# Kernel optimization log

Hardware: AMD Instinct MI355X
Metric: run time of the kernel (lower is better)

## Reference

```python
import jax, jax.numpy as jnp
import numpy as np

B, N, D = 8, 2048, 512


def setup_inputs() -> dict:
    key = jax.random.key(0)
    ks = jax.random.split(key, 16)
    s = 1.0 / np.sqrt(D)  # ~ torch Linear default init scale
    inp = {
        "X": jax.random.normal(ks[0], (B, N, D), jnp.float32),
        "Y": jax.random.normal(ks[1], (B, N, D), jnp.float32),
    }
    names = ["xq", "xk", "xv", "yq", "yk", "yv"]
    for i, nm in enumerate(names):
        inp[f"W_{nm}"] = jax.random.uniform(ks[2 + 2 * i], (D, D), jnp.float32, -s, s)
        inp[f"b_{nm}"] = jax.random.uniform(ks[3 + 2 * i], (D,), jnp.float32, -s, s)
    return inp


def _lin(x, W, b):
    # torch nn.Linear: x @ W^T + b
    return jnp.einsum("bnd,ed->bne", x, W) + b


def reference(X, Y, W_xq, b_xq, W_xk, b_xk, W_xv, b_xv, W_yq, b_yq, W_yk, b_yk, W_yv, b_yv):
    d = X.shape[-1]
    scale = 1.0 / jnp.sqrt(jnp.asarray(d, X.dtype))
    Q1, K1, V1 = _lin(X, W_xq, b_xq), _lin(X, W_xk, b_xk), _lin(X, W_xv, b_xv)
    Q2, K2, V2 = _lin(Y, W_yq, b_yq), _lin(Y, W_yk, b_yk), _lin(Y, W_yv, b_yv)
    # NOTE: F.softmax called without dim on a 3-D tensor -> torch legacy dim=0 (batch axis).
    S1 = jnp.einsum("bnd,bmd->bnm", Q1, K2) * scale  # [B, N, N]
    A1 = jax.nn.softmax(S1, axis=0)
    U_A1 = X + jnp.einsum("bnm,bmd->bnd", A1, V2)  # dropout = identity (eval)
    S2 = jnp.einsum("bnd,bmd->bnm", Q2, K1) * scale
    A2 = jax.nn.softmax(S2, axis=0)
    U_A2 = Y + jnp.einsum("bnm,bmd->bnd", A2, V1)
    return U_A1 + U_A2
```

## Files before the change

### kernel.cpp

```cpp
#include <hip/hip_runtime.h>

typedef unsigned short u16;
typedef unsigned char u8;
typedef __attribute__((ext_vector_type(8))) short bf16x8;
typedef __attribute__((ext_vector_type(4))) float f32x4;
typedef __attribute__((ext_vector_type(8))) u16 u16x8;
typedef __attribute__((ext_vector_type(2))) int i32x2;
typedef __attribute__((ext_vector_type(2))) float f32x2;

#define GLOAD_LDS(g, s) __builtin_amdgcn_global_load_lds( \
    (const __attribute__((address_space(1))) void*)(g),   \
    (__attribute__((address_space(3))) void*)(s), 16, 0, 0)

__device__ __forceinline__ u16 f2bf(float f) {
  union { float f; unsigned u; } v; v.f = f;
  unsigned r = v.u + 0x7fffu + ((v.u >> 16) & 1u);
  return (u16)(r >> 16);
}
__device__ __forceinline__ float bf2f(u16 h) {
  union { unsigned u; float f; } v; v.u = ((unsigned)h) << 16;
  return v.f;
}

__device__ __forceinline__ unsigned lds_addr(const void* p) {
  return (unsigned)(unsigned long long)(__attribute__((address_space(3))) const void*)p;
}
__device__ __forceinline__ bf16x8 ds128(const void* p) {
  bf16x8 r;
  asm volatile("ds_read_b128 %0, %1" : "=v"(r) : "v"(lds_addr(p)));
  return r;
}
__device__ __forceinline__ i32x2 ds64(const void* p) {
  i32x2 r;
  asm volatile("ds_read_b64 %0, %1" : "=v"(r) : "v"(lds_addr(p)));
  return r;
}
__device__ __forceinline__ bf16x8 cvt8(i32x2 v) {
  f32x2 f0 = __builtin_amdgcn_cvt_pk_f32_fp8(v[0], false);
  f32x2 f1 = __builtin_amdgcn_cvt_pk_f32_fp8(v[0], true);
  f32x2 f2 = __builtin_amdgcn_cvt_pk_f32_fp8(v[1], false);
  f32x2 f3 = __builtin_amdgcn_cvt_pk_f32_fp8(v[1], true);
  unsigned w0, w1, w2, w3;
  asm("v_cvt_pk_bf16_f32 %0, %1, %2" : "=v"(w0) : "v"(f0[0]), "v"(f0[1]));
  asm("v_cvt_pk_bf16_f32 %0, %1, %2" : "=v"(w1) : "v"(f1[0]), "v"(f1[1]));
  asm("v_cvt_pk_bf16_f32 %0, %1, %2" : "=v"(w2) : "v"(f2[0]), "v"(f2[1]));
  asm("v_cvt_pk_bf16_f32 %0, %1, %2" : "=v"(w3) : "v"(f3[0]), "v"(f3[1]));
  union { unsigned w[4]; bf16x8 v8; } u;
  u.w[0] = w0; u.w[1] = w1; u.w[2] = w2; u.w[3] = w3;
  return u.v8;
}

__device__ __forceinline__ void stage_pair(const u16* gA, int lda, const u16* gB, int ldb,
                                           u16* lA, u16* lB, int wave, int lane) {
  int row = (wave << 4) + (lane >> 2);
  int kb  = (lane & 3) << 3;
  GLOAD_LDS(gA + row * lda + kb,        lA + (wave << 9));
  GLOAD_LDS(gA + (row + 64) * lda + kb, lA + ((wave + 4) << 9));
  GLOAD_LDS(gB + row * ldb + kb,        lB + (wave << 9));
  GLOAD_LDS(gB + (row + 64) * ldb + kb, lB + ((wave + 4) << 9));
}

__device__ __forceinline__ void gemm_seg(f32x4 (&acc)[4][4],
    const u16* Ag, const u16* Bg, int lda, int ldb, int nk,
    u16* As, u16* Bs, int wave, int lane) {
  const int wr = (wave >> 1) << 6, wc = (wave & 1) << 6;
  const int rl = lane & 15, rk = (lane >> 4) << 3;
  stage_pair(Ag, lda, Bg, ldb, As, Bs, wave, lane);
  if (nk > 1)
    stage_pair(Ag + 32, lda, Bg + 32, ldb, As + 4096, Bs + 4096, wave, lane);
  int bufsel = 0;
  for (int kt = 0; kt < nk; ++kt) {
    if (kt + 1 < nk) asm volatile("s_waitcnt vmcnt(4)" ::: "memory");
    else             asm volatile("s_waitcnt vmcnt(0)" ::: "memory");
    __builtin_amdgcn_s_barrier();
    asm volatile("" ::: "memory");
    if (kt + 2 < nk) {
      int nb = bufsel + 2; if (nb >= 3) nb -= 3;
      stage_pair(Ag + (long)(kt + 2) * 32, lda, Bg + (long)(kt + 2) * 32, ldb,
                 As + nb * 4096, Bs + nb * 4096, wave, lane);
    }
    const u16* ab = As + bufsel * 4096;
    const u16* bb = Bs + bufsel * 4096;
    bf16x8 af[4], bfr[4];
#pragma unroll
    for (int i = 0; i < 4; i++)
      af[i]  = *(const bf16x8*)(ab + ((wr + (i << 4) + rl) << 5) + rk);
#pragma unroll
    for (int j = 0; j < 4; j++)
      bfr[j] = *(const bf16x8*)(bb + ((wc + (j << 4) + rl) << 5) + rk);
#pragma unroll
    for (int i = 0; i < 4; i++)
#pragma unroll
      for (int j = 0; j < 4; j++)
        acc[i][j] = __builtin_amdgcn_mfma_f32_16x16x32_bf16(af[i], bfr[j], acc[i][j], 0, 0, 0);
    __builtin_amdgcn_sched_barrier(0);
    bufsel = bufsel + 1; if (bufsel == 3) bufsel = 0;
  }
}

__device__ __forceinline__ void stage_one(const u16* g, int ld, u16* d, int tid) {
  int rw = tid >> 3;
  int gs = ((tid & 7) ^ (rw & 7)) << 3;
  int wb = (tid >> 6) << 9;
#pragma unroll
  for (int p = 0; p < 4; p++)
    GLOAD_LDS(g + (long)(p * 64 + rw) * ld + gs, d + p * 4096 + wb);
}

__device__ __forceinline__ void gemm256d(f32x4 (&acc)[8][4],
    const u16* Ag, int lda, const u16* Bg, int ldb, int nk,
    u16* As, u16* Bs, int tid) {
  const int lane = tid & 63, wid = tid >> 6;
  const int wr = (wid >> 2) << 7;
  const int wc = (wid & 3) << 6;
  const int rl = lane & 15, kg = lane >> 4;
  const int swz0 = (kg ^ (rl & 7)) << 3;
  const int rbA = (wr + rl) * 64, rbB = (wc + rl) * 64;

  stage_one(Ag, lda, As, tid);
  stage_one(Bg, ldb, Bs, tid);
  if (nk > 1) stage_one(Ag + 64, lda, As + 16384, tid);

  int ba = 0;
  for (int t = 0; t < nk; ++t) {
    if (t + 1 < nk) asm volatile("s_waitcnt vmcnt(4)" ::: "memory");
    else            asm volatile("s_waitcnt vmcnt(0)" ::: "memory");
    __builtin_amdgcn_s_barrier();
    if (t + 1 < nk)
      stage_one(Bg + (t + 1) * 64, ldb, Bs + ((t + 1) & 1) * 16384, tid);
    if (t + 2 < nk) {
      int nb = ba + 2; if (nb >= 3) nb -= 3;
      stage_one(Ag + (long)(t + 2) * 64, lda, As + nb * 16384, tid);
    }
    const u16* ab = As + ba * 16384 + rbA;
    const u16* bb = Bs + (t & 1) * 16384 + rbB;
#pragma unroll
    for (int kk = 0; kk < 2; kk++) {
      const int sw = swz0 ^ (kk << 5);
      bf16x8 a[8], b[4];
#pragma unroll
      for (int i = 0; i < 8; i++) a[i] = ds128(ab + i * 1024 + sw);
#pragma unroll
      for (int j = 0; j < 4; j++) b[j] = ds128(bb + j * 1024 + sw);
      asm volatile("s_waitcnt lgkmcnt(0)" ::: "memory");
      __builtin_amdgcn_sched_barrier(0);
      __builtin_amdgcn_s_setprio(1);
#pragma unroll
      for (int i = 0; i < 8; i++)
#pragma unroll
        for (int j = 0; j < 4; j++)
          acc[i][j] = __builtin_amdgcn_mfma_f32_16x16x32_bf16(a[i], b[j], acc[i][j], 0, 0, 0);
      __builtin_amdgcn_s_setprio(0);
      __builtin_amdgcn_sched_barrier(0);
    }
    ba = ba + 1; if (ba == 3) ba = 0;
  }
}

__device__ __forceinline__ void stage_pv(const u8* gA, const u16* gB,
                                         u8* Ad, u8* Bd, int tid) {
  int w = tid >> 6;
#pragma unroll
  for (int pass = 0; pass < 2; pass++) {
    int gid = pass * 512 + tid;
    int ra = gid >> 2, ga = gid & 3;
    GLOAD_LDS(gA + (long)ra * 2048 + ((ga ^ (ra & 3)) << 4),
              Ad + pass * 8192 + w * 1024);
    int rb = gid >> 3, gb = gid & 7;
    GLOAD_LDS(gB + (long)rb * 2048 + ((gb ^ (rb & 7)) << 3),
              Bd + pass * 8192 + w * 1024);
  }
}

__device__ __forceinline__ void gemm_pv8(f32x4 (&acc)[4][4],
    const u8* Ag, const u16* Bg, u8* As, u8* Bs, int tid) {
  const int lane = tid & 63, wid = tid >> 6;
  const int mq = wid >> 1, nh = wid & 1;
  const int rl = lane & 15, kg = lane >> 4;
  const int nk = 32;

  stage_pv(Ag, Bg, As, Bs, tid);
  stage_pv(Ag + 64, Bg + 64, As + 16384, Bs + 16384, tid);
  int bsel = 0;
  for (int t = 0; t < nk; ++t) {
    if (t + 1 < nk) asm volatile("s_waitcnt vmcnt(4)" ::: "memory");
    else            asm volatile("s_waitcnt vmcnt(0)" ::: "memory");
    __builtin_amdgcn_s_barrier();
    if (t + 2 < nk) {
      int nb = bsel + 2; if (nb >= 3) nb -= 3;
      stage_pv(Ag + (long)(t + 2) * 64, Bg + (t + 2) * 64,
               As + nb * 16384, Bs + nb * 16384, tid);
    }
    const u8* ab = As + bsel * 16384 + (mq * 64 + rl) * 64 + ((kg & 1) << 3);
    const u8* bb = Bs + bsel * 16384 + (nh * 64 + rl) * 128;
#pragma unroll
    for (int kk = 0; kk < 2; kk++) {
      const int sa = (((kk << 1) + (kg >> 1)) ^ (rl & 3)) << 4;
      const int sb = (((kk << 2) + kg) ^ (rl & 7)) << 4;
      i32x2 ar[4]; bf16x8 bfr[4];
#pragma unroll
      for (int i = 0; i < 4; i++) ar[i] = ds64(ab + i * 1024 + sa);
#pragma unroll
      for (int j = 0; j < 4; j++) bfr[j] = ds128(bb + j * 2048 + sb);
      asm volatile("s_waitcnt lgkmcnt(0)" ::: "memory");
      __builtin_amdgcn_sched_barrier(0);
      bf16x8 a[4];
#pragma unroll
      for (int i = 0; i < 4; i++) a[i] = cvt8(ar[i]);
      __builtin_amdgcn_s_setprio(1);
#pragma unroll
      for (int i = 0; i < 4; i++)
#pragma unroll
        for (int j = 0; j < 4; j++)
          acc[i][j] = __builtin_amdgcn_mfma_f32_16x16x32_bf16(a[i], bfr[j], acc[i][j], 0, 0, 0);
      __builtin_amdgcn_s_setprio(0);
      __builtin_amdgcn_sched_barrier(0);
    }
    bsel = bsel + 1; if (bsel == 3) bsel = 0;
  }
}

__global__ __launch_bounds__(256) void k_cvt2(const float* __restrict__ inX,
                                              const float* __restrict__ inY,
                                              u16* __restrict__ oX, u16* __restrict__ oY,
                                              int n8) {
  int i = blockIdx.x * 256 + threadIdx.x;
  const float* in = (i < n8) ? inX : inY;
  u16* out = (i < n8) ? oX : oY;
  int k = (i < n8) ? i : i - n8;
  const float4* pf = (const float4*)in + (long)k * 2;
  float4 a = pf[0], b = pf[1];
  u16x8 o;
  o[0] = f2bf(a.x); o[1] = f2bf(a.y); o[2] = f2bf(a.z); o[3] = f2bf(a.w);
  o[4] = f2bf(b.x); o[5] = f2bf(b.y); o[6] = f2bf(b.z); o[7] = f2bf(b.w);
  *((u16x8*)out + k) = o;
}

struct P6 { const float* p[6]; };
struct O6 { u16* p[6]; };

__global__ __launch_bounds__(256) void k_cvt_w(P6 w, u16* __restrict__ out) {
  int z = blockIdx.y;
  int i = blockIdx.x * 256 + threadIdx.x;
  const float4* pf = (const float4*)w.p[z] + (long)i * 2;
  float4 a = pf[0], b = pf[1];
  u16x8 o;
  o[0] = f2bf(a.x); o[1] = f2bf(a.y); o[2] = f2bf(a.z); o[3] = f2bf(a.w);
  o[4] = f2bf(b.x); o[5] = f2bf(b.y); o[6] = f2bf(b.z); o[7] = f2bf(b.w);
  *((u16x8*)(out + (long)z * 262144) + i) = o;
}

__global__ __launch_bounds__(256) void k_proj(const u16* __restrict__ Xb, const u16* __restrict__ Yb,
                                              const u16* __restrict__ Wb, P6 bias, O6 dst) {
  __shared__ u16 As[12288], Bs[12288];
  int x = blockIdx.x;
  int swz = (x & 7) * 384 + (x >> 3);
  int bm = swz / 24;
  int r  = swz - bm * 24;
  int z = r >> 2, bn = r & 3;
  int tid = threadIdx.x, wave = tid >> 6, lane = tid & 63;
  const u16* Ag = (z < 3 ? Xb : Yb) + (long)bm * 128 * 512;
  const u16* Bg = Wb + (long)z * 262144 + (long)bn * 128 * 512;
  f32x4 acc[4][4] = {};
  gemm_seg(acc, Ag, Bg, 512, 512, 16, As, Bs, wave, lane);
  const float* bi = bias.p[z];
  u16* D = dst.p[z];
  int wr = (wave >> 1) << 6, wc = (wave & 1) << 6;
  int row0 = bm * 128 + wr + ((lane >> 4) << 2);
  int col0 = bn * 128 + wc + (lane & 15);
  float bj[4];
#pragma unroll
  for (int j = 0; j < 4; j++) bj[j] = bi[col0 + (j << 4)];
#pragma unroll
  for (int i = 0; i < 4; i++)
#pragma unroll
    for (int j = 0; j < 4; j++)
#pragma unroll
      for (int rr = 0; rr < 4; rr++)
        D[(long)(row0 + (i << 4) + rr) * 512 + col0 + (j << 4)] = f2bf(acc[i][j][rr] + bj[j]);
}

__global__ __launch_bounds__(512) void k_s(const u16* __restrict__ Q, const u16* __restrict__ K,
                                           u16* __restrict__ S) {
  __shared__ u16 As[49152], Bs[32768];
  int x = blockIdx.x;
  int swz = (x & 7) * 64 + (x >> 3);
  int bn = swz & 7, bm = (swz >> 3) & 7, b = swz >> 6;
  int tid = threadIdx.x;
  const u16* Ag = Q + (long)b * 1048576 + (long)bm * 256 * 512;
  const u16* Bg = K + (long)b * 1048576 + (long)bn * 256 * 512;
  f32x4 acc[8][4] = {};
  gemm256d(acc, Ag, 512, Bg, 512, 8, As, Bs, tid);
  u16* D = S + (long)b * 4194304;
  const float scale = 0.04419417382415922f;
  int lane = tid & 63, wid = tid >> 6;
  int row0 = bm * 256 + ((wid >> 2) << 7) + ((lane >> 4) << 2);
  int col0 = bn * 256 + ((wid & 3) << 6) + (lane & 15);
#pragma unroll
  for (int i = 0; i < 8; i++)
#pragma unroll
    for (int j = 0; j < 4; j++)
#pragma unroll
      for (int rr = 0; rr < 4; rr++)
        D[(long)(row0 + (i << 4) + rr) * 2048 + col0 + (j << 4)] = f2bf(acc[i][j][rr] * scale);
}

__global__ __launch_bounds__(256) void k_softmax8(const u16* __restrict__ S,
                                                  u8* __restrict__ A8) {
  int idx = blockIdx.x * 256 + threadIdx.x;
  u16x8 v[8];
#pragma unroll
  for (int b = 0; b < 8; b++) v[b] = *((const u16x8*)(S + (long)b * 4194304) + idx);
  unsigned w0[8], w1[8];
#pragma unroll
  for (int jp = 0; jp < 4; jp++) {
    float va[8], vb[8];
    {
      float e[8], m = -1e30f;
#pragma unroll
      for (int b = 0; b < 8; b++) { e[b] = bf2f(v[b][2 * jp]); m = fmaxf(m, e[b]); }
      float s = 0.f;
#pragma unroll
      for (int b = 0; b < 8; b++) { e[b] = __expf(e[b] - m); s += e[b]; }
      float inv = 1.0f / s;
#pragma unroll
      for (int b = 0; b < 8; b++) va[b] = e[b] * inv;
    }
    {
      float e[8], m = -1e30f;
#pragma unroll
      for (int b = 0; b < 8; b++) { e[b] = bf2f(v[b][2 * jp + 1]); m = fmaxf(m, e[b]); }
      float s = 0.f;
#pragma unroll
      for (int b = 0; b < 8; b++) { e[b] = __expf(e[b] - m); s += e[b]; }
      float inv = 1.0f / s;
#pragma unroll
      for (int b = 0; b < 8; b++) vb[b] = e[b] * inv;
    }
#pragma unroll
    for (int b = 0; b < 8; b++) {
      if (jp == 0)      w0[b] = __builtin_amdgcn_cvt_pk_fp8_f32(va[b], vb[b], 0,     false);
      else if (jp == 1) w0[b] = __builtin_amdgcn_cvt_pk_fp8_f32(va[b], vb[b], w0[b], true);
      else if (jp == 2) w1[b] = __builtin_amdgcn_cvt_pk_fp8_f32(va[b], vb[b], 0,     false);
      else              w1[b] = __builtin_amdgcn_cvt_pk_fp8_f32(va[b], vb[b], w1[b], true);
    }
  }
#pragma unroll
  for (int b = 0; b < 8; b++) {
    i32x2 w; w[0] = (int)w0[b]; w[1] = (int)w1[b];
    *(i32x2*)(A8 + (long)b * 4194304 + (long)idx * 8) = w;
  }
}

__global__ __launch_bounds__(256) void k_tr(const u16* __restrict__ V1, const u16* __restrict__ V2,
                                            u16* __restrict__ T1, u16* __restrict__ T2) {
  __shared__ u16 tile[64][65];
  int z = blockIdx.z;
  const u16* src = (z < 8 ? V1 : V2) + (long)(z & 7) * 1048576;
  u16*       dst = (z < 8 ? T1 : T2) + (long)(z & 7) * 1048576;
  int n0 = blockIdx.x * 64, d0 = blockIdx.y * 64;
  int t = threadIdx.x;
  int r = t >> 2, cs = (t & 3) * 16;
  const u16x8* sp = (const u16x8*)(src + (long)(n0 + r) * 512 + d0 + cs);
  u16x8 a = sp[0], b = sp[1];
#pragma unroll
  for (int jj = 0; jj < 8; jj++) { tile[r][cs + jj] = a[jj]; tile[r][cs + 8 + jj] = b[jj]; }
  __syncthreads();
  u16x8 o0, o1;
#pragma unroll
  for (int jj = 0; jj < 8; jj++) { o0[jj] = tile[cs + jj][r]; o1[jj] = tile[cs + 8 + jj][r]; }
  u16x8* op = (u16x8*)(dst + (long)(d0 + r) * 2048 + n0 + cs);
  op[0] = o0; op[1] = o1;
}

__global__ __launch_bounds__(512) void k_pv8(const u8* __restrict__ A8, const u16* __restrict__ Vt,
                                             const float* __restrict__ X, const float* __restrict__ Y,
                                             float* __restrict__ out, int mode) {
  __shared__ u8 As[49152], Bs[49152];
  int x = blockIdx.x;
  int swz = (x & 7) * 32 + (x >> 3);
  int bn = swz & 3, bm = (swz >> 2) & 7, b = swz >> 5;
  int tid = threadIdx.x;
  const u8*  Ag = A8 + (long)b * 4194304 + (long)bm * 256 * 2048;
  const u16* Bg = Vt + (long)b * 1048576 + (long)bn * 128 * 2048;
  f32x4 acc[4][4] = {};
  gemm_pv8(acc, Ag, Bg, As, Bs, tid);
  int lane = tid & 63, wid = tid >> 6;
  int mq = wid >> 1, nh = wid & 1;
  int row0 = bm * 256 + mq * 64 + ((lane >> 4) << 2);
  int col0 = bn * 128 + nh * 64 + (lane & 15);
  long base = (long)b * 1048576;
#pragma unroll
  for (int i = 0; i < 4; i++)
#pragma unroll
    for (int j = 0; j < 4; j++)
#pragma unroll
      for (int rr = 0; rr < 4; rr++) {
        long idx = base + (long)(row0 + (i << 4) + rr) * 512 + col0 + (j << 4);
        float v = acc[i][j][rr];
        out[idx] = mode ? (out[idx] + v) : (v + X[idx] + Y[idx]);
      }
}

extern "C" void kernel_launch(void* const* d_in, const int* in_sizes, int n_in,
                              void* d_out, int out_size, void* d_ws, size_t ws_size,
                              hipStream_t stream) {
  const float* X = (const float*)d_in[0];
  const float* Y = (const float*)d_in[1];
  P6 wp, bp;
  for (int i = 0; i < 6; i++) { wp.p[i] = (const float*)d_in[2 + 2 * i]; bp.p[i] = (const float*)d_in[3 + 2 * i]; }

  const long NX = 8L * 2048 * 512;
  const long NS = 8L * 2048 * 2048;
  u16* p = (u16*)d_ws;
  u16* Xb = p;  p += NX;
  u16* Yb = p;  p += NX;
  u16* Wb = p;  p += 6L * 512 * 512;
  u16* Q1 = p;  p += NX;
  u16* K2 = p;  p += NX;
  u16* Q2 = p;  p += NX;
  u16* K1 = p;  p += NX;
  u16* Sb = p;  p += NS;
  u16* V1 = Sb;
  u16* V2 = Sb + NX;
  u16* Vt1 = Xb;
  u16* Vt2 = Yb;
  u8* A8_2 = (u8*)Q2;
  u8* A8_1 = (u8*)Q1;
  (void)ws_size; (void)in_sizes; (void)n_in; (void)out_size;

  dim3 T(256);
  k_cvt2<<<dim3(8192), T, 0, stream>>>(X, Y, Xb, Yb, (int)(NX / 8));
  k_cvt_w<<<dim3(128, 6), T, 0, stream>>>(wp, Wb);
  O6 dst; dst.p[0] = Q1; dst.p[1] = K1; dst.p[2] = V1; dst.p[3] = Q2; dst.p[4] = K2; dst.p[5] = V2;
  k_proj<<<dim3(3072), T, 0, stream>>>(Xb, Yb, Wb, bp, dst);
  k_tr<<<dim3(32, 8, 16), T, 0, stream>>>(V1, V2, Vt1, Vt2);
  k_s<<<dim3(512), dim3(512), 0, stream>>>(Q2, K1, Sb);
  k_softmax8<<<dim3(2048), T, 0, stream>>>(Sb, A8_2);
  k_pv8<<<dim3(256), dim3(512), 0, stream>>>(A8_2, Vt1, X, Y, (float*)d_out, 0);
  k_s<<<dim3(512), dim3(512), 0, stream>>>(Q1, K2, Sb);
  k_softmax8<<<dim3(2048), T, 0, stream>>>(Sb, A8_1);
  k_pv8<<<dim3(256), dim3(512), 0, stream>>>(A8_1, Vt2, X, Y, (float*)d_out, 1);
}
```

Measured before the change: 342.3 us.

## Double the PV K-tile and software-pipeline LDS fragment loads in gemm_pv8

The PV GEMM now stages 128-wide K tiles instead of 64, halving the number of main-loop barriers. The fp8 A tile stays triple-buffered, while the V tile moves to double buffering with its own staging call. Inside each K step, LDS fragment reads for the next sub-step are issued before the MFMAs of the current one (register double buffering with a partial lgkmcnt wait), to hide LDS latency. Shared memory grows to 160 KB per block, which limits occupancy to one block per CU, and the vmcnt(4) accounting now has to match a different number of outstanding loads.

```diff
diff --git a/kernel.cpp b/kernel.cpp
--- a/kernel.cpp
+++ b/kernel.cpp
@@ -157,18 +157,20 @@
   }
 }
 
-__device__ __forceinline__ void stage_pv(const u8* gA, const u16* gB,
-                                         u8* Ad, u8* Bd, int tid) {
-  int w = tid >> 6;
-#pragma unroll
-  for (int pass = 0; pass < 2; pass++) {
+__device__ __forceinline__ void stage_A8(const u8* gA, u8* Ad, int tid) {
+#pragma unroll
+  for (int pass = 0; pass < 4; pass++) {
     int gid = pass * 512 + tid;
-    int ra = gid >> 2, ga = gid & 3;
-    GLOAD_LDS(gA + (long)ra * 2048 + ((ga ^ (ra & 3)) << 4),
-              Ad + pass * 8192 + w * 1024);
-    int rb = gid >> 3, gb = gid & 7;
-    GLOAD_LDS(gB + (long)rb * 2048 + ((gb ^ (rb & 7)) << 3),
-              Bd + pass * 8192 + w * 1024);
+    int row = gid >> 3, g = gid & 7;
+    GLOAD_LDS(gA + (long)row * 2048 + ((g ^ (row & 7)) << 4), Ad + (gid << 4));
+  }
+}
+__device__ __forceinline__ void stage_Bv(const u16* gB, u8* Bd, int tid) {
+#pragma unroll
+  for (int pass = 0; pass < 4; pass++) {
+    int gid = pass * 512 + tid;
+    int row = gid >> 4, g = gid & 15;
+    GLOAD_LDS(gB + (long)row * 2048 + ((g ^ (row & 7)) << 3), Bd + (gid << 4));
   }
 }
 
@@ -177,46 +179,62 @@
   const int lane = tid & 63, wid = tid >> 6;
   const int mq = wid >> 1, nh = wid & 1;
   const int rl = lane & 15, kg = lane >> 4;
-  const int nk = 32;
-
-  stage_pv(Ag, Bg, As, Bs, tid);
-  stage_pv(Ag + 64, Bg + 64, As + 16384, Bs + 16384, tid);
-  int bsel = 0;
+  const int nk = 16;
+  const int abase = (mq * 64 + rl) * 128 + ((kg & 1) << 3);
+  const int bbase = (nh * 64 + rl) * 256;
+
+  stage_A8(Ag, As, tid);
+  stage_Bv(Bg, Bs, tid);
+  stage_A8(Ag + 128, As + 32768, tid);
+  int ba = 0;
   for (int t = 0; t < nk; ++t) {
     if (t + 1 < nk) asm volatile("s_waitcnt vmcnt(4)" ::: "memory");
     else            asm volatile("s_waitcnt vmcnt(0)" ::: "memory");
     __builtin_amdgcn_s_barrier();
+    if (t + 1 < nk) stage_Bv(Bg + (t + 1) * 128, Bs + ((t + 1) & 1) * 32768, tid);
     if (t + 2 < nk) {
-      int nb = bsel + 2; if (nb >= 3) nb -= 3;
-      stage_pv(Ag + (long)(t + 2) * 64, Bg + (t + 2) * 64,
-               As + nb * 16384, Bs + nb * 16384, tid);
-    }
-    const u8* ab = As + bsel * 16384 + (mq * 64 + rl) * 64 + ((kg & 1) << 3);
-    const u8* bb = Bs + bsel * 16384 + (nh * 64 + rl) * 128;
-#pragma unroll
-    for (int kk = 0; kk < 2; kk++) {
-      const int sa = (((kk << 1) + (kg >> 1)) ^ (rl & 3)) << 4;
-      const int sb = (((kk << 2) + kg) ^ (rl & 7)) << 4;
-      i32x2 ar[4]; bf16x8 bfr[4];
-#pragma unroll
-      for (int i = 0; i < 4; i++) ar[i] = ds64(ab + i * 1024 + sa);
-#pragma unroll
-      for (int j = 0; j < 4; j++) bfr[j] = ds128(bb + j * 2048 + sb);
-      asm volatile("s_waitcnt lgkmcnt(0)" ::: "memory");
+      int nb = ba + 2; if (nb >= 3) nb -= 3;
+      stage_A8(Ag + (long)(t + 2) * 128, As + nb * 32768, tid);
+    }
+    const u8* ab = As + ba * 32768 + abase;
+    const u8* bb = Bs + (t & 1) * 32768 + bbase;
+    i32x2 ar[2][4]; bf16x8 br[2][4];
+    {
+      const int sa = ((kg >> 1) ^ (rl & 7)) << 4;
+      const int sb = (kg ^ (rl & 7)) << 4;
+#pragma unroll
+      for (int i = 0; i < 4; i++) ar[0][i] = ds64(ab + i * 2048 + sa);
+#pragma unroll
+      for (int j = 0; j < 4; j++) br[0][j] = ds128(bb + j * 4096 + sb);
+    }
+#pragma unroll
+    for (int kk = 0; kk < 4; kk++) {
+      const int cu = kk & 1, nx = cu ^ 1;
+      if (kk < 3) {
+        const int sa = ((((kk + 1) << 1) + (kg >> 1)) ^ (rl & 7)) << 4;
+        const int sb = ((((kk + 1) << 2) + kg) ^ (rl & 7)) << 4;
+#pragma unroll
+        for (int i = 0; i < 4; i++) ar[nx][i] = ds64(ab + i * 2048 + sa);
+#pragma unroll
+        for (int j = 0; j < 4; j++) br[nx][j] = ds128(bb + j * 4096 + sb);
+        asm volatile("s_waitcnt lgkmcnt(8)" ::: "memory");
+      } else {
+        asm volatile("s_waitcnt lgkmcnt(0)" ::: "memory");
+      }
       __builtin_amdgcn_sched_barrier(0);
       bf16x8 a[4];
 #pragma unroll
-      for (int i = 0; i < 4; i++) a[i] = cvt8(ar[i]);
+      for (int i = 0; i < 4; i++) a[i] = cvt8(ar[cu][i]);
       __builtin_amdgcn_s_setprio(1);
 #pragma unroll
       for (int i = 0; i < 4; i++)
 #pragma unroll
         for (int j = 0; j < 4; j++)
-          acc[i][j] = __builtin_amdgcn_mfma_f32_16x16x32_bf16(a[i], bfr[j], acc[i][j], 0, 0, 0);
+          acc[i][j] = __builtin_amdgcn_mfma_f32_16x16x32_bf16(a[i], br[cu][j], acc[i][j], 0, 0, 0);
       __builtin_amdgcn_s_setprio(0);
       __builtin_amdgcn_sched_barrier(0);
     }
-    bsel = bsel + 1; if (bsel == 3) bsel = 0;
+    ba = ba + 1; if (ba == 3) ba = 0;
   }
 }
 
@@ -376,7 +394,7 @@
 __global__ __launch_bounds__(512) void k_pv8(const u8* __restrict__ A8, const u16* __restrict__ Vt,
                                              const float* __restrict__ X, const float* __restrict__ Y,
                                              float* __restrict__ out, int mode) {
-  __shared__ u8 As[49152], Bs[49152];
+  __shared__ u8 As[98304], Bs[65536];
   int x = blockIdx.x;
   int swz = (x & 7) * 32 + (x >> 3);
   int bn = swz & 3, bm = (swz >> 2) & 7, b = swz >> 5;
```

Measured after the change: 343.9 us. About the same (+0.5%).

## Merge both PV GEMMs into one split-K kernel with a reduction pass

Applied to the files above, without the earlier changes.

The two separate PV launches (A2·V1 and A1·V2) are replaced by one kernel that accumulates both products in the same registers. The K dimension is split in two across blocks, giving 512 blocks instead of 256 for better CU occupancy. Partial sums for the second K half go to a scratch buffer that aliases the score buffer, and a small elementwise kernel adds them in afterwards. LDS staging is also restructured: A keeps triple buffering, B drops to double buffering, and the LDS footprint shrinks. The costs are an extra fp32 partial write and read plus one more launch.

```diff
diff --git a/kernel.cpp b/kernel.cpp
--- a/kernel.cpp
+++ b/kernel.cpp
@@ -157,18 +157,20 @@
   }
 }
 
-__device__ __forceinline__ void stage_pv(const u8* gA, const u16* gB,
-                                         u8* Ad, u8* Bd, int tid) {
-  int w = tid >> 6;
+__device__ __forceinline__ void stage_A64(const u8* gA, u8* Ad, int tid) {
 #pragma unroll
   for (int pass = 0; pass < 2; pass++) {
     int gid = pass * 512 + tid;
-    int ra = gid >> 2, ga = gid & 3;
-    GLOAD_LDS(gA + (long)ra * 2048 + ((ga ^ (ra & 3)) << 4),
-              Ad + pass * 8192 + w * 1024);
-    int rb = gid >> 3, gb = gid & 7;
-    GLOAD_LDS(gB + (long)rb * 2048 + ((gb ^ (rb & 7)) << 3),
-              Bd + pass * 8192 + w * 1024);
+    int row = gid >> 2, g = gid & 3;
+    GLOAD_LDS(gA + (long)row * 2048 + ((g ^ (row & 3)) << 4), Ad + (gid << 4));
+  }
+}
+__device__ __forceinline__ void stage_B64(const u16* gB, u8* Bd, int tid) {
+#pragma unroll
+  for (int pass = 0; pass < 2; pass++) {
+    int gid = pass * 512 + tid;
+    int row = gid >> 3, g = gid & 7;
+    GLOAD_LDS(gB + (long)row * 2048 + ((g ^ (row & 7)) << 3), Bd + (gid << 4));
   }
 }
 
@@ -177,22 +179,25 @@
   const int lane = tid & 63, wid = tid >> 6;
   const int mq = wid >> 1, nh = wid & 1;
   const int rl = lane & 15, kg = lane >> 4;
-  const int nk = 32;
-
-  stage_pv(Ag, Bg, As, Bs, tid);
-  stage_pv(Ag + 64, Bg + 64, As + 16384, Bs + 16384, tid);
-  int bsel = 0;
+  const int nk = 16;
+  const int abase = (mq * 64 + rl) * 64 + ((kg & 1) << 3);
+  const int bbase = (nh * 64 + rl) * 128;
+
+  stage_A64(Ag, As, tid);
+  stage_B64(Bg, Bs, tid);
+  stage_A64(Ag + 64, As + 16384, tid);
+  int ba = 0;
   for (int t = 0; t < nk; ++t) {
-    if (t + 1 < nk) asm volatile("s_waitcnt vmcnt(4)" ::: "memory");
+    if (t + 1 < nk) asm volatile("s_waitcnt vmcnt(2)" ::: "memory");
     else            asm volatile("s_waitcnt vmcnt(0)" ::: "memory");
     __builtin_amdgcn_s_barrier();
+    if (t + 1 < nk) stage_B64(Bg + (t + 1) * 64, Bs + ((t + 1) & 1) * 16384, tid);
     if (t + 2 < nk) {
-      int nb = bsel + 2; if (nb >= 3) nb -= 3;
-      stage_pv(Ag + (long)(t + 2) * 64, Bg + (t + 2) * 64,
-               As + nb * 16384, Bs + nb * 16384, tid);
-    }
-    const u8* ab = As + bsel * 16384 + (mq * 64 + rl) * 64 + ((kg & 1) << 3);
-    const u8* bb = Bs + bsel * 16384 + (nh * 64 + rl) * 128;
+      int nb = ba + 2; if (nb >= 3) nb -= 3;
+      stage_A64(Ag + (long)(t + 2) * 64, As + nb * 16384, tid);
+    }
+    const u8* ab = As + ba * 16384 + abase;
+    const u8* bb = Bs + (t & 1) * 16384 + bbase;
 #pragma unroll
     for (int kk = 0; kk < 2; kk++) {
       const int sa = (((kk << 1) + (kg >> 1)) ^ (rl & 3)) << 4;
@@ -216,7 +221,7 @@
       __builtin_amdgcn_s_setprio(0);
       __builtin_amdgcn_sched_barrier(0);
     }
-    bsel = bsel + 1; if (bsel == 3) bsel = 0;
+    ba = ba + 1; if (ba == 3) ba = 0;
   }
 }
 
@@ -373,18 +378,23 @@
   op[0] = o0; op[1] = o1;
 }
 
-__global__ __launch_bounds__(512) void k_pv8(const u8* __restrict__ A8, const u16* __restrict__ Vt,
-                                             const float* __restrict__ X, const float* __restrict__ Y,
-                                             float* __restrict__ out, int mode) {
-  __shared__ u8 As[49152], Bs[49152];
+__global__ __launch_bounds__(512) void k_pv8m(const u8* __restrict__ A2, const u16* __restrict__ Vt1,
+                                              const u8* __restrict__ A1, const u16* __restrict__ Vt2,
+                                              const float* __restrict__ X, const float* __restrict__ Y,
+                                              float* __restrict__ out, float* __restrict__ P) {
+  __shared__ u8 As[49152], Bs[32768];
   int x = blockIdx.x;
-  int swz = (x & 7) * 32 + (x >> 3);
-  int bn = swz & 3, bm = (swz >> 2) & 7, b = swz >> 5;
+  int swz = (x & 7) * 64 + (x >> 3);
+  int b = swz >> 6;
+  int r = swz & 63;
+  int bn = r & 3, kc = (r >> 2) & 1, bm = r >> 3;
   int tid = threadIdx.x;
-  const u8*  Ag = A8 + (long)b * 4194304 + (long)bm * 256 * 2048;
-  const u16* Bg = Vt + (long)b * 1048576 + (long)bn * 128 * 2048;
+  long aoff = (long)b * 4194304 + (long)bm * 256 * 2048 + kc * 1024;
+  long voff = (long)b * 1048576 + (long)bn * 128 * 2048 + kc * 1024;
   f32x4 acc[4][4] = {};
-  gemm_pv8(acc, Ag, Bg, As, Bs, tid);
+  gemm_pv8(acc, A2 + aoff, Vt1 + voff, As, Bs, tid);
+  __builtin_amdgcn_s_barrier();
+  gemm_pv8(acc, A1 + aoff, Vt2 + voff, As, Bs, tid);
   int lane = tid & 63, wid = tid >> 6;
   int mq = wid >> 1, nh = wid & 1;
   int row0 = bm * 256 + mq * 64 + ((lane >> 4) << 2);
@@ -398,8 +408,17 @@
       for (int rr = 0; rr < 4; rr++) {
         long idx = base + (long)(row0 + (i << 4) + rr) * 512 + col0 + (j << 4);
         float v = acc[i][j][rr];
-        out[idx] = mode ? (out[idx] + v) : (v + X[idx] + Y[idx]);
+        if (kc) P[idx] = v;
+        else    out[idx] = v + X[idx] + Y[idx];
       }
+}
+
+__global__ __launch_bounds__(256) void k_fin(float* __restrict__ out, const float* __restrict__ P) {
+  long i = (long)(blockIdx.x * 256 + threadIdx.x) * 4;
+  float4 o = *(const float4*)(out + i);
+  float4 p = *(const float4*)(P + i);
+  o.x += p.x; o.y += p.y; o.z += p.z; o.w += p.w;
+  *(float4*)(out + i) = o;
 }
 
 extern "C" void kernel_launch(void* const* d_in, const int* in_sizes, int n_in,
@@ -427,6 +446,7 @@
   u16* Vt2 = Yb;
   u8* A8_2 = (u8*)Q2;
   u8* A8_1 = (u8*)Q1;
+  float* Pbuf = (float*)Sb;
   (void)ws_size; (void)in_sizes; (void)n_in; (void)out_size;
 
   dim3 T(256);
@@ -437,8 +457,8 @@
   k_tr<<<dim3(32, 8, 16), T, 0, stream>>>(V1, V2, Vt1, Vt2);
   k_s<<<dim3(512), dim3(512), 0, stream>>>(Q2, K1, Sb);
   k_softmax8<<<dim3(2048), T, 0, stream>>>(Sb, A8_2);
-  k_pv8<<<dim3(256), dim3(512), 0, stream>>>(A8_2, Vt1, X, Y, (float*)d_out, 0);
   k_s<<<dim3(512), dim3(512), 0, stream>>>(Q1, K2, Sb);
   k_softmax8<<<dim3(2048), T, 0, stream>>>(Sb, A8_1);
-  k_pv8<<<dim3(256), dim3(512), 0, stream>>>(A8_1, Vt2, X, Y, (float*)d_out, 1);
-}
+  k_pv8m<<<dim3(512), dim3(512), 0, stream>>>(A8_2, Vt1, A8_1, Vt2, X, Y, (float*)d_out, Pbuf);
+  k_fin<<<dim3((int)(NX / 1024)), T, 0, stream>>>((float*)d_out, Pbuf);
+}
```

Measured after the change: 343.0 us. Within noise of the previous version (+0.2%).
